# Performance work log

Measured on AMD Instinct MI355X. Metric: run time of the kernel, lower is better.

Reference implementation:

```python
import jax, jax.numpy as jnp
from jax import lax
import numpy as np

B, T, K = 256, 1024, 128


def setup_inputs() -> dict:
    key = jax.random.key(0)
    k1, k2, k3 = jax.random.split(key, 3)
    inputs = jax.random.normal(k1, (B, T, K), dtype=jnp.float32)
    transitions = jax.random.normal(k2, (K, K), dtype=jnp.float32)
    tags = jax.random.randint(k3, (B, T), 0, K, dtype=jnp.int64)
    mask = jnp.ones((B, T), dtype=jnp.int32)
    return {"inputs": inputs, "transitions": transitions, "tags": tags, "mask": mask}


def _input_likelihood(inputs, transitions, maskf):
    # inputs: [B,T,K] emissions; forward algorithm (no start/end transitions)
    emit = jnp.transpose(inputs, (1, 0, 2))  # [T,B,K]
    m = jnp.transpose(maskf, (1, 0))         # [T,B]
    alpha0 = emit[0]                          # [B,K]

    def step(alpha, xm):
        e, mi = xm  # e: [B,K], mi: [B]
        # inner[b,i,j] = alpha[b,i] + transitions[i,j] + e[b,j]
        inner = alpha[:, :, None] + transitions[None, :, :] + e[:, None, :]
        new = jax.nn.logsumexp(inner, axis=1)  # [B,K]
        alpha = new * mi[:, None] + alpha * (1.0 - mi[:, None])
        return alpha, None

    alpha, _ = lax.scan(step, alpha0, (emit[1:], m[1:]))
    return jax.nn.logsumexp(alpha, axis=-1)  # [B]


def _joint_likelihood(inputs, transitions, tags, mask, maskf):
    b, t, k = inputs.shape
    # transition scores between consecutive gold tags
    trans_scores = transitions[tags[:, :-1], tags[:, 1:]]              # [B,T-1]
    # emission scores at gold tags
    emit_scores = jnp.take_along_axis(inputs, tags[..., None], axis=2)[..., 0]  # [B,T]
    score = jnp.sum(trans_scores * maskf[:, 1:], axis=-1) \
          + jnp.sum(emit_scores[:, :-1] * maskf[:, :-1], axis=-1)
    # last valid tag's emission at the final timestep (AllenNLP semantics)
    last_idx = jnp.sum(mask, axis=1).astype(jnp.int32) - 1             # [B]
    last_tags = jnp.take_along_axis(tags, last_idx[:, None].astype(tags.dtype), axis=1)[:, 0]
    last_input_score = jnp.take_along_axis(inputs[:, -1, :], last_tags[:, None], axis=1)[:, 0]
    score = score + last_input_score * maskf[:, -1]
    return score  # [B]


def reference(inputs, transitions, tags, mask):
    maskf = mask.astype(inputs.dtype)
    log_denominator = _input_likelihood(inputs, transitions, maskf)
    log_numerator = _joint_likelihood(inputs, transitions, tags, mask, maskf)
    loglik = log_numerator - log_denominator
    return jnp.sum(loglik)  # reduction='sum'
```

## Files before the change

### kernel.cpp

```cpp
#include <hip/hip_runtime.h>
#include <math.h>

#define BB 256
#define TT 1024
#define KK 128
#define CHUNK 8
#define NCHUNK (TT / CHUNK)
#define PHALF 80
#define PIDX(i) ((i) + (((i) >> 6) << 4))

__global__ void zero_out_kernel(float* out) { out[0] = 0.0f; }

__global__ __launch_bounds__(256, 1) void crf_kernel(
    const float* __restrict__ inputs,
    const float* __restrict__ trans,
    const int* __restrict__ tags,
    const int* __restrict__ mask,
    float* __restrict__ out)
{
    __shared__ __align__(16) float pbuf[2][2 * PHALF];
    __shared__ __align__(16) float ebuf[2][CHUNK * KK];
    __shared__ float mbuf[2][CHUNK];
    __shared__ float scratch[8];

    const int tid = threadIdx.x;
    const int q   = tid & 1;
    const int j   = tid >> 1;
    const int b   = blockIdx.x;

    const float* binp = inputs + (size_t)b * TT * KK;
    const int* bmask  = mask + (size_t)b * TT;
    const int* btags  = tags + (size_t)b * TT;

    float4 E[16];
#pragma unroll
    for (int c4 = 0; c4 < 16; ++c4) {
        const float* tp = trans + (size_t)(q * 64 + 4 * c4) * KK + j;
        E[c4].x = expf(tp[0 * KK]);
        E[c4].y = expf(tp[1 * KK]);
        E[c4].z = expf(tp[2 * KK]);
        E[c4].w = expf(tp[3 * KK]);
    }

    {
        float4 e4 = ((const float4*)binp)[tid];
        e4.x = __expf(e4.x); e4.y = __expf(e4.y);
        e4.z = __expf(e4.z); e4.w = __expf(e4.w);
        ((float4*)ebuf[0])[tid] = e4;
    }
    if (tid < CHUNK) mbuf[0][tid] = (float)bmask[tid];
    __syncthreads();

    float pcur = ebuf[0][j];
    int m_int = 0;
    if (q == 0) pbuf[0][PIDX(j)] = pcur;
    __syncthreads();

    for (int c = 0; c < NCHUNK; ++c) {
        float4 epre; int mpre = 0;
        if (c + 1 < NCHUNK) {
            epre = ((const float4*)(binp + (size_t)(c + 1) * CHUNK * KK))[tid];
            if (tid < CHUNK) mpre = bmask[(c + 1) * CHUNK + tid];
        }
        const float* eb = ebuf[c & 1];
        const float* mb = mbuf[c & 1];
        const int s0 = (c == 0) ? 1 : 0;
        for (int s = s0; s < CHUNK; ++s) {
            const int t = c * CHUNK + s;
            const float* pr = pbuf[(t - 1) & 1] + q * PHALF;
            float4 pv0 = ((const float4*)pr)[0];
            float z0 = pv0.x * E[0].x;
            float z1 = pv0.y * E[0].y;
            float z2 = pv0.z * E[0].z;
            float z3 = pv0.w * E[0].w;
#pragma unroll
            for (int c4 = 1; c4 < 16; ++c4) {
                float4 pv = ((const float4*)pr)[c4];
                z0 = fmaf(pv.x, E[c4].x, z0);
                z1 = fmaf(pv.y, E[c4].y, z1);
                z2 = fmaf(pv.z, E[c4].z, z2);
                z3 = fmaf(pv.w, E[c4].w, z3);
            }
            float z = (z0 + z1) + (z2 + z3);
            z += __shfl_xor(z, 1);
            float X  = eb[s * KK + j];
            float mi = mb[s];
            float pn = (mi != 0.0f) ? z * X : pcur;
            int E0 = (int)((__float_as_uint(pv0.x) >> 23) & 255u) - 127;
            float sc = __uint_as_float((unsigned)(127 - E0) << 23);
            pcur = pn * sc;
            m_int += E0;
            if (q == 0) pbuf[t & 1][PIDX(j)] = pcur;
            __syncthreads();
        }
        if (c + 1 < NCHUNK) {
            epre.x = __expf(epre.x); epre.y = __expf(epre.y);
            epre.z = __expf(epre.z); epre.w = __expf(epre.w);
            ((float4*)ebuf[(c + 1) & 1])[tid] = epre;
            if (tid < CHUNK) mbuf[(c + 1) & 1][tid] = (float)mpre;
            __syncthreads();
        }
    }

    float a = (q == 0) ? ((float)m_int * 0.69314718055994531f + logf(pcur))
                       : -INFINITY;
    float v = a;
#pragma unroll
    for (int o = 1; o < 64; o <<= 1) v = fmaxf(v, __shfl_xor(v, o));
    if ((tid & 63) == 0) scratch[tid >> 6] = v;
    __syncthreads();
    float mx = fmaxf(fmaxf(scratch[0], scratch[1]), fmaxf(scratch[2], scratch[3]));
    float ev = (q == 0) ? __expf(a - mx) : 0.0f;
#pragma unroll
    for (int o = 1; o < 64; o <<= 1) ev += __shfl_xor(ev, o);
    __syncthreads();
    if ((tid & 63) == 0) scratch[tid >> 6] = ev;
    __syncthreads();
    float den = mx + logf((scratch[0] + scratch[1]) + (scratch[2] + scratch[3]));

    float numpart = 0.0f, maskpart = 0.0f;
#pragma unroll
    for (int kk = 0; kk < TT / 256; ++kk) {
        int t = tid + 256 * kk;
        int tg = btags[t];
        float mf = (float)bmask[t];
        maskpart += mf;
        if (t < TT - 1) {
            int tg1   = btags[t + 1];
            float mf1 = (float)bmask[t + 1];
            numpart += trans[tg * KK + tg1] * mf1;
            numpart += binp[(size_t)t * KK + tg] * mf;
        }
    }
#pragma unroll
    for (int o = 1; o < 64; o <<= 1) numpart += __shfl_xor(numpart, o);
#pragma unroll
    for (int o = 1; o < 64; o <<= 1) maskpart += __shfl_xor(maskpart, o);
    __syncthreads();
    if ((tid & 63) == 0) {
        scratch[tid >> 6]       = numpart;
        scratch[4 + (tid >> 6)] = maskpart;
    }
    __syncthreads();
    if (tid == 0) {
        float num  = (scratch[0] + scratch[1]) + (scratch[2] + scratch[3]);
        float msum = (scratch[4] + scratch[5]) + (scratch[6] + scratch[7]);
        int last_idx = (int)msum - 1;
        int ltag = btags[last_idx];
        num += binp[(size_t)(TT - 1) * KK + ltag] * (float)bmask[TT - 1];
        atomicAdd(out, num - den);
    }
}

extern "C" void kernel_launch(void* const* d_in, const int* in_sizes, int n_in,
                              void* d_out, int out_size, void* d_ws, size_t ws_size,
                              hipStream_t stream) {
    const float* inputs = (const float*)d_in[0];
    const float* trans  = (const float*)d_in[1];
    const int* tagsp    = (const int*)d_in[2];
    const int* maskp    = (const int*)d_in[3];
    float* out          = (float*)d_out;
    zero_out_kernel<<<1, 1, 0, stream>>>(out);
    crf_kernel<<<BB, 256, 0, stream>>>(inputs, trans, tagsp, maskp, out);
}
```

Before: 720.7 us.

## Use one thread per tag with packed FMA, dropping the pair split and shuffle

Each block now runs 128 threads, so every thread owns one output tag and all 128 transition weights sit in registers as float2 pairs, accumulated with packed v2f FMAs. This removes the per-step cross-lane shuffle and halves the threads reaching each barrier, in exchange for twice the FMA work per thread and higher register pressure. The padded split layout of the shared alpha buffer is replaced by a plain 128-entry array that all lanes broadcast-read.

```diff
diff --git a/kernel.cpp b/kernel.cpp
--- a/kernel.cpp
+++ b/kernel.cpp
@@ -6,60 +6,60 @@
 #define KK 128
 #define CHUNK 8
 #define NCHUNK (TT / CHUNK)
-#define PHALF 80
-#define PIDX(i) ((i) + (((i) >> 6) << 4))
+
+typedef float v2f __attribute__((ext_vector_type(2)));
 
 __global__ void zero_out_kernel(float* out) { out[0] = 0.0f; }
 
-__global__ __launch_bounds__(256, 1) void crf_kernel(
+__global__ __launch_bounds__(128) void crf_kernel(
     const float* __restrict__ inputs,
     const float* __restrict__ trans,
     const int* __restrict__ tags,
     const int* __restrict__ mask,
     float* __restrict__ out)
 {
-    __shared__ __align__(16) float pbuf[2][2 * PHALF];
+    __shared__ __align__(16) float pbuf[2][KK];
     __shared__ __align__(16) float ebuf[2][CHUNK * KK];
     __shared__ float mbuf[2][CHUNK];
-    __shared__ float scratch[8];
+    __shared__ float sred[4];
 
     const int tid = threadIdx.x;
-    const int q   = tid & 1;
-    const int j   = tid >> 1;
     const int b   = blockIdx.x;
 
     const float* binp = inputs + (size_t)b * TT * KK;
     const int* bmask  = mask + (size_t)b * TT;
     const int* btags  = tags + (size_t)b * TT;
 
-    float4 E[16];
+    const float* tcol = trans + tid;
+    v2f E2[64];
 #pragma unroll
-    for (int c4 = 0; c4 < 16; ++c4) {
-        const float* tp = trans + (size_t)(q * 64 + 4 * c4) * KK + j;
-        E[c4].x = expf(tp[0 * KK]);
-        E[c4].y = expf(tp[1 * KK]);
-        E[c4].z = expf(tp[2 * KK]);
-        E[c4].w = expf(tp[3 * KK]);
+    for (int k = 0; k < 64; ++k) {
+        E2[k].x = expf(tcol[(size_t)(2 * k) * KK]);
+        E2[k].y = expf(tcol[(size_t)(2 * k + 1) * KK]);
     }
 
     {
-        float4 e4 = ((const float4*)binp)[tid];
-        e4.x = __expf(e4.x); e4.y = __expf(e4.y);
-        e4.z = __expf(e4.z); e4.w = __expf(e4.w);
-        ((float4*)ebuf[0])[tid] = e4;
+        float4 e0 = ((const float4*)binp)[tid];
+        float4 e1 = ((const float4*)binp)[tid + 128];
+        e0.x = __expf(e0.x); e0.y = __expf(e0.y); e0.z = __expf(e0.z); e0.w = __expf(e0.w);
+        e1.x = __expf(e1.x); e1.y = __expf(e1.y); e1.z = __expf(e1.z); e1.w = __expf(e1.w);
+        ((float4*)ebuf[0])[tid]       = e0;
+        ((float4*)ebuf[0])[tid + 128] = e1;
     }
     if (tid < CHUNK) mbuf[0][tid] = (float)bmask[tid];
     __syncthreads();
 
-    float pcur = ebuf[0][j];
+    float pcur = ebuf[0][tid];
     int m_int = 0;
-    if (q == 0) pbuf[0][PIDX(j)] = pcur;
+    pbuf[0][tid] = pcur;
     __syncthreads();
 
     for (int c = 0; c < NCHUNK; ++c) {
-        float4 epre; int mpre = 0;
+        float4 ep0, ep1; int mpre = 0;
         if (c + 1 < NCHUNK) {
-            epre = ((const float4*)(binp + (size_t)(c + 1) * CHUNK * KK))[tid];
+            const float4* src = (const float4*)(binp + (size_t)(c + 1) * CHUNK * KK);
+            ep0 = src[tid];
+            ep1 = src[tid + 128];
             if (tid < CHUNK) mpre = bmask[(c + 1) * CHUNK + tid];
         }
         const float* eb = ebuf[c & 1];
@@ -67,61 +67,66 @@
         const int s0 = (c == 0) ? 1 : 0;
         for (int s = s0; s < CHUNK; ++s) {
             const int t = c * CHUNK + s;
-            const float* pr = pbuf[(t - 1) & 1] + q * PHALF;
-            float4 pv0 = ((const float4*)pr)[0];
-            float z0 = pv0.x * E[0].x;
-            float z1 = pv0.y * E[0].y;
-            float z2 = pv0.z * E[0].z;
-            float z3 = pv0.w * E[0].w;
+            const float4* pr4 = (const float4*)pbuf[(t - 1) & 1];
+            float X  = eb[s * KK + tid];
+            float mi = mb[s];
+            float p00;
+            v2f za = {0.f, 0.f}, zb = {0.f, 0.f}, zc = {0.f, 0.f}, zd = {0.f, 0.f};
 #pragma unroll
-            for (int c4 = 1; c4 < 16; ++c4) {
-                float4 pv = ((const float4*)pr)[c4];
-                z0 = fmaf(pv.x, E[c4].x, z0);
-                z1 = fmaf(pv.y, E[c4].y, z1);
-                z2 = fmaf(pv.z, E[c4].z, z2);
-                z3 = fmaf(pv.w, E[c4].w, z3);
+            for (int r = 0; r < 8; ++r) {
+                float4 pa = pr4[4 * r + 0];
+                float4 pb = pr4[4 * r + 1];
+                float4 pc = pr4[4 * r + 2];
+                float4 pd = pr4[4 * r + 3];
+                if (r == 0) p00 = pa.x;
+                za = __builtin_elementwise_fma((v2f){pa.x, pa.y}, E2[8 * r + 0], za);
+                zb = __builtin_elementwise_fma((v2f){pa.z, pa.w}, E2[8 * r + 1], zb);
+                zc = __builtin_elementwise_fma((v2f){pb.x, pb.y}, E2[8 * r + 2], zc);
+                zd = __builtin_elementwise_fma((v2f){pb.z, pb.w}, E2[8 * r + 3], zd);
+                za = __builtin_elementwise_fma((v2f){pc.x, pc.y}, E2[8 * r + 4], za);
+                zb = __builtin_elementwise_fma((v2f){pc.z, pc.w}, E2[8 * r + 5], zb);
+                zc = __builtin_elementwise_fma((v2f){pd.x, pd.y}, E2[8 * r + 6], zc);
+                zd = __builtin_elementwise_fma((v2f){pd.z, pd.w}, E2[8 * r + 7], zd);
             }
-            float z = (z0 + z1) + (z2 + z3);
-            z += __shfl_xor(z, 1);
-            float X  = eb[s * KK + j];
-            float mi = mb[s];
+            v2f zz = (za + zb) + (zc + zd);
+            float z = zz.x + zz.y;
             float pn = (mi != 0.0f) ? z * X : pcur;
-            int E0 = (int)((__float_as_uint(pv0.x) >> 23) & 255u) - 127;
+            int E0 = (int)((__float_as_uint(p00) >> 23) & 255u) - 127;
             float sc = __uint_as_float((unsigned)(127 - E0) << 23);
             pcur = pn * sc;
             m_int += E0;
-            if (q == 0) pbuf[t & 1][PIDX(j)] = pcur;
+            pbuf[t & 1][tid] = pcur;
             __syncthreads();
         }
         if (c + 1 < NCHUNK) {
-            epre.x = __expf(epre.x); epre.y = __expf(epre.y);
-            epre.z = __expf(epre.z); epre.w = __expf(epre.w);
-            ((float4*)ebuf[(c + 1) & 1])[tid] = epre;
+            ep0.x = __expf(ep0.x); ep0.y = __expf(ep0.y); ep0.z = __expf(ep0.z); ep0.w = __expf(ep0.w);
+            ep1.x = __expf(ep1.x); ep1.y = __expf(ep1.y); ep1.z = __expf(ep1.z); ep1.w = __expf(ep1.w);
+            ((float4*)ebuf[(c + 1) & 1])[tid]       = ep0;
+            ((float4*)ebuf[(c + 1) & 1])[tid + 128] = ep1;
             if (tid < CHUNK) mbuf[(c + 1) & 1][tid] = (float)mpre;
             __syncthreads();
         }
     }
 
-    float a = (q == 0) ? ((float)m_int * 0.69314718055994531f + logf(pcur))
-                       : -INFINITY;
+    float a = (float)m_int * 0.69314718055994531f + logf(pcur);
     float v = a;
 #pragma unroll
     for (int o = 1; o < 64; o <<= 1) v = fmaxf(v, __shfl_xor(v, o));
-    if ((tid & 63) == 0) scratch[tid >> 6] = v;
+    if ((tid & 63) == 0) sred[tid >> 6] = v;
     __syncthreads();
-    float mx = fmaxf(fmaxf(scratch[0], scratch[1]), fmaxf(scratch[2], scratch[3]));
-    float ev = (q == 0) ? __expf(a - mx) : 0.0f;
+    float mx = fmaxf(sred[0], sred[1]);
+    float ev = __expf(a - mx);
 #pragma unroll
     for (int o = 1; o < 64; o <<= 1) ev += __shfl_xor(ev, o);
     __syncthreads();
-    if ((tid & 63) == 0) scratch[tid >> 6] = ev;
+    if ((tid & 63) == 0) sred[tid >> 6] = ev;
     __syncthreads();
-    float den = mx + logf((scratch[0] + scratch[1]) + (scratch[2] + scratch[3]));
+    float den = mx + logf(sred[0] + sred[1]);
 
     float numpart = 0.0f, maskpart = 0.0f;
 #pragma unroll
-    for (int kk = 0; kk < TT / 256; ++kk) {
-        int t = tid + 256 * kk;
+    for (int kk = 0; kk < TT / 128; ++kk) {
+        int t = tid + 128 * kk;
         int tg = btags[t];
         float mf = (float)bmask[t];
         maskpart += mf;
@@ -138,13 +143,13 @@
     for (int o = 1; o < 64; o <<= 1) maskpart += __shfl_xor(maskpart, o);
     __syncthreads();
     if ((tid & 63) == 0) {
-        scratch[tid >> 6]       = numpart;
-        scratch[4 + (tid >> 6)] = maskpart;
+        sred[tid >> 6]     = numpart;
+        sred[2 + (tid >> 6)] = maskpart;
     }
     __syncthreads();
     if (tid == 0) {
-        float num  = (scratch[0] + scratch[1]) + (scratch[2] + scratch[3]);
-        float msum = (scratch[4] + scratch[5]) + (scratch[6] + scratch[7]);
+        float num  = sred[0] + sred[1];
+        float msum = sred[2] + sred[3];
         int last_idx = (int)msum - 1;
         int ltag = btags[last_idx];
         num += binp[(size_t)(TT - 1) * KK + ltag] * (float)bmask[TT - 1];
@@ -161,5 +166,5 @@
     const int* maskp    = (const int*)d_in[3];
     float* out          = (float*)d_out;
     zero_out_kernel<<<1, 1, 0, stream>>>(out);
-    crf_kernel<<<BB, 256, 0, stream>>>(inputs, trans, tagsp, maskp, out);
+    crf_kernel<<<BB, 128, 0, stream>>>(inputs, trans, tagsp, maskp, out);
 }
```

Measured after the change: 693.7 us. -3.7%, faster.
